# Kernel tuning notes

Measured on AMD Instinct MI355X. Metric: run time of the kernel, lower is better.

Reference implementation:

```python
import jax, jax.numpy as jnp
import numpy as np

B, N, C, E, H, V, T = 64, 196, 512, 512, 1024, 10000, 20
NULL_IDX, START_IDX = 0, 1


def setup_inputs() -> dict:
    key = jax.random.key(0)
    ks = jax.random.split(key, 16)
    p = lambda k, s: jax.random.normal(k, s, jnp.float32) * 0.02
    z = lambda n: jnp.zeros((n,), jnp.float32)
    return dict(
        X=jax.random.normal(ks[0], (B, N, C), jnp.float32),
        emb=p(ks[1], (V, E)),
        W_ih=p(ks[2], (E + C, 4 * H)), b_ih=z(4 * H),
        W_hh=p(ks[3], (H, 4 * H)), b_hh=z(4 * H),
        Wa=p(ks[4], (C, H)), ba=z(H),          # attention lin_annotations
        Wh=p(ks[5], (H, H)), bh=z(H),          # attention lin_hidden
        Wo=p(ks[6], (H, 1)), bo=z(1),          # attention out
        Wlh=p(ks[7], (H, E)), blh=z(E),        # linear_hidden
        Wlc=p(ks[8], (C, E)), blc=z(E),        # linear_context
        Wout=p(ks[9], (E, V)), bout=z(V),      # linear_out
        Wc0=p(ks[10], (C, H)), bc0=z(H),       # cell_init
        Wh0=p(ks[11], (C, H)), bh0=z(H),       # hidden_init
    )


def reference(X, emb, W_ih, b_ih, W_hh, b_hh, Wa, ba, Wh, bh, Wo, bo,
              Wlh, blh, Wlc, blc, Wout, bout, Wc0, bc0, Wh0, bh0):
    Xm = jnp.mean(X, axis=1)                       # [B, C]
    c0 = jnp.tanh(Xm @ Wc0 + bc0)                  # [B, H]
    h0 = jnp.tanh(Xm @ Wh0 + bh0)                  # [B, H]
    Xa = X @ Wa + ba                               # [B, N, H] step-invariant annotation proj
    tok0 = jnp.full((B,), START_IDX, jnp.int32)

    def step(carry, _):
        tok, h, c = carry
        e = emb[tok]                                           # [B, E]
        att = jnp.tanh(Xa + (h @ Wh + bh)[:, None, :])          # [B, N, H]
        # softmax over a size-1 last axis -> weights == 1 (faithful to original)
        w = jax.nn.softmax(att @ Wo + bo, axis=-1)              # [B, N, 1]
        ctx = jnp.sum(w * X, axis=1)                            # [B, C]
        gates = jnp.concatenate([e, ctx], axis=1) @ W_ih + b_ih + h @ W_hh + b_hh
        gi, gf, gg, go = jnp.split(gates, 4, axis=1)            # torch LSTMCell gate order
        c2 = jax.nn.sigmoid(gf) * c + jax.nn.sigmoid(gi) * jnp.tanh(gg)
        h2 = jax.nn.sigmoid(go) * jnp.tanh(c2)
        comb = e + (h2 @ Wlh + blh) + (ctx @ Wlc + blc)         # [B, E]
        lp = jax.nn.log_softmax(comb @ Wout + bout, axis=-1)    # [B, V]
        tok2 = jnp.argmax(lp, axis=-1).astype(jnp.int32)
        return (tok2, h2, c2), lp

    _, lps = jax.lax.scan(step, (tok0, h0, c0), None, length=T - 1)  # [T-1, B, V]
    out0 = jnp.broadcast_to(jax.nn.one_hot(START_IDX, V, dtype=jnp.float32), (B, V))[None]
    out = jnp.concatenate([out0, lps], axis=0)                  # [T, B, V]
    return jnp.transpose(out, (1, 0, 2))                        # [B, T, V]
```

## Files before the change

kernel.cpp:

```cpp
#include <hip/hip_runtime.h>
#include <math.h>

typedef unsigned short u16;
typedef unsigned long long u64;
typedef __attribute__((ext_vector_type(8))) short bf16x8;
typedef __attribute__((ext_vector_type(4))) float f32x4;
typedef __attribute__((ext_vector_type(8))) unsigned short ushort8;

constexpr int kB = 64;
constexpr int kN = 196;
constexpr int kC = 512;
constexpr int kE = 512;
constexpr int kH = 1024;
constexpr int kV = 10000;
constexpr int kT = 20;
constexpr int kG4 = 4 * kH;
constexpr int kKA = 1536;
constexpr int kLT = 625;

__device__ __forceinline__ float sigmoidf_(float x) { return 1.0f / (1.0f + expf(-x)); }

__device__ __forceinline__ u16 f2bf(float x) {
    unsigned u = __float_as_uint(x);
    u += 0x7FFF + ((u >> 16) & 1);
    return (u16)(u >> 16);
}
__device__ __forceinline__ float bf2f(u16 u) {
    return __uint_as_float((unsigned)u << 16);
}
__device__ __forceinline__ void splitbf(float x, u16& hi, u16& lo) {
    hi = f2bf(x);
    lo = f2bf(x - bf2f(hi));
}

__device__ __forceinline__ u64 packMI(float M, int I) {
    unsigned mb = __float_as_uint(M);
    mb = (mb & 0x80000000u) ? ~mb : (mb | 0x80000000u);
    return ((u64)mb << 32) | (u64)(0xFFFFFFFFu - (unsigned)I);
}


__global__ __launch_bounds__(256) void k_colsum(const float* __restrict__ X,
                                                float* __restrict__ XsP) {
    int gid = blockIdx.x * 256 + threadIdx.x;
    int c = gid & 511, b = (gid >> 9) & 63, ch = gid >> 15;
    const float* p = X + (size_t)b * kN * kC + (size_t)(ch * 49) * kC + c;
    float s = 0.f;
    for (int n = 0; n < 49; ++n) s += p[(size_t)n * kC];
    XsP[gid] = s;
}

__global__ __launch_bounds__(256) void k_colred(const float* __restrict__ XsP,
                                                float* __restrict__ XsT) {
    int gid = blockIdx.x * 256 + threadIdx.x;
    int b = gid >> 9, c = gid & 511;
    float s = 0.f;
#pragma unroll
    for (int ch = 0; ch < 4; ++ch) s += XsP[ch * 32768 + b * 512 + c];
    XsT[c * kB + b] = s;
}

__global__ __launch_bounds__(256) void k_setupgemm(const float* __restrict__ XsT,
                                                   const float* __restrict__ W_ih,
                                                   const float* __restrict__ b_ih,
                                                   const float* __restrict__ b_hh,
                                                   const float* __restrict__ Wc0,
                                                   const float* __restrict__ bc0,
                                                   const float* __restrict__ Wh0,
                                                   const float* __restrict__ bh0,
                                                   const float* __restrict__ Wlc,
                                                   const float* __restrict__ blc,
                                                   const float* __restrict__ blh,
                                                   float* __restrict__ gbP,
                                                   float* __restrict__ cBJ,
                                                   u16* __restrict__ hb0Hi,
                                                   u16* __restrict__ hb0Lo,
                                                   float* __restrict__ ctxc) {
    __shared__ float4 wt4[64][8];
    int t = threadIdx.x;
    int b = t & 63, q = t >> 6;
    int tile = blockIdx.x;

    const float* W; const float* bias; float scale; int ldw; int mode; int j;
    if (tile < 128) {
        j = tile * 32; W = W_ih + (size_t)kE * kG4 + j; ldw = kG4;
        bias = nullptr; scale = 1.f; mode = 0;
    } else if (tile < 160) {
        j = (tile - 128) * 32; W = Wc0 + j; ldw = kH;
        bias = bc0 + j; scale = 1.0f / 196.0f; mode = 1;
    } else if (tile < 192) {
        j = (tile - 160) * 32; W = Wh0 + j; ldw = kH;
        bias = bh0 + j; scale = 1.0f / 196.0f; mode = 2;
    } else {
        j = (tile - 192) * 32; W = Wlc + j; ldw = kE;
        bias = blc + j; scale = 1.f; mode = 3;
    }

    int lr = t >> 2, lq2 = (t & 3) * 2;
    float acc[8];
#pragma unroll
    for (int i = 0; i < 8; ++i) acc[i] = 0.f;

    for (int kt = 0; kt < kC; kt += 64) {
        const float* wrow = W + (size_t)(kt + lr) * ldw;
        float4 w0 = *reinterpret_cast<const float4*>(wrow + lq2 * 4);
        float4 w1 = *reinterpret_cast<const float4*>(wrow + lq2 * 4 + 4);
        __syncthreads();
        wt4[lr][lq2] = w0; wt4[lr][lq2 + 1] = w1;
        __syncthreads();
        const float* ap = XsT + (size_t)kt * kB + b;
#pragma unroll 8
        for (int kk = 0; kk < 64; ++kk) {
            float a = ap[kk * 64] * scale;
            float4 u0 = wt4[kk][q * 2];
            float4 u1 = wt4[kk][q * 2 + 1];
            acc[0] += a * u0.x; acc[1] += a * u0.y; acc[2] += a * u0.z; acc[3] += a * u0.w;
            acc[4] += a * u1.x; acc[5] += a * u1.y; acc[6] += a * u1.z; acc[7] += a * u1.w;
        }
    }
#pragma unroll
    for (int cc = 0; cc < 8; ++cc) {
        int col = q * 8 + cc;
        float v = acc[cc];
        if (mode == 0) {
            int jsrc = j + col;
            v += b_ih[jsrc] + b_hh[jsrc];
            int nd = ((jsrc & 1023) << 2) | (jsrc >> 10);
            gbP[(size_t)b * kG4 + nd] = v;
        } else if (mode == 1) {
            v = tanhf(v + bias[col]);
            cBJ[(size_t)b * kH + j + col] = v;
        } else if (mode == 2) {
            v = tanhf(v + bias[col]);
            u16 hi, lo; splitbf(v, hi, lo);
            hb0Hi[(size_t)b * kH + j + col] = hi;
            hb0Lo[(size_t)b * kH + j + col] = lo;
        } else {
            v += bias[col] + blh[j + col];
            ctxc[(size_t)b * kE + j + col] = v;
        }
    }
}

__global__ __launch_bounds__(256) void k_wconv(const float* __restrict__ src,
                                               u16* __restrict__ dhi,
                                               u16* __restrict__ dlo,
                                               int ld, int n_valid, int pitch,
                                               int k_off, int nxTiles) {
    __shared__ float lds[64][65];
    int t = threadIdx.x;
    int nx = blockIdx.x % nxTiles, ky = blockIdx.x / nxTiles;
    int n0 = nx * 64, k0 = ky * 64;
    int c = t & 63, r0 = t >> 6;
#pragma unroll
    for (int i = 0; i < 16; ++i) {
        int r = r0 + i * 4;
        float v = (n0 + c < n_valid) ? src[(size_t)(k0 + r) * ld + n0 + c] : 0.f;
        lds[r][c] = v;
    }
    __syncthreads();
    int nl = t >> 2, kq = t & 3;
#pragma unroll
    for (int half = 0; half < 2; ++half) {
        ushort8 vh, vl;
#pragma unroll
        for (int jj = 0; jj < 8; ++jj) {
            u16 hi, lo; splitbf(lds[kq * 16 + half * 8 + jj][nl], hi, lo);
            vh[jj] = hi; vl[jj] = lo;
        }
        size_t o = (size_t)(n0 + nl) * pitch + k_off + k0 + kq * 16 + half * 8;
        *(ushort8*)(&dhi[o]) = vh;
        *(ushort8*)(&dlo[o]) = vl;
    }
}

__global__ __launch_bounds__(256) void k_wgconv(const float* __restrict__ src,
                                                u16* __restrict__ dhi,
                                                int k_off) {
    __shared__ float lds[64][65];
    int t = threadIdx.x;
    int nx = blockIdx.x & 63, ky = blockIdx.x >> 6;
    int n0 = nx * 64, k0 = ky * 64;
    int c = t & 63, r0 = t >> 6;
#pragma unroll
    for (int i = 0; i < 16; ++i) {
        int r = r0 + i * 4;
        int nd = n0 + c;
        int nsrc = (nd & 3) * 1024 + (nd >> 2);
        lds[r][c] = src[(size_t)(k0 + r) * kG4 + nsrc];
    }
    __syncthreads();
    int nl = t >> 2, kq = t & 3;
#pragma unroll
    for (int half = 0; half < 2; ++half) {
        ushort8 vh;
#pragma unroll
        for (int jj = 0; jj < 8; ++jj) vh[jj] = f2bf(lds[kq * 16 + half * 8 + jj][nl]);
        size_t o = (size_t)(n0 + nl) * kKA + k_off + k0 + kq * 16 + half * 8;
        *(ushort8*)(&dhi[o]) = vh;
    }
}

__global__ __launch_bounds__(256) void k_wconvh(const float* __restrict__ src,
                                                u16* __restrict__ dhi,
                                                int ld, int pitch, int nxTiles) {
    __shared__ float lds[64][65];
    int t = threadIdx.x;
    int nx = blockIdx.x % nxTiles, ky = blockIdx.x / nxTiles;
    int n0 = nx * 64, k0 = ky * 64;
    int c = t & 63, r0 = t >> 6;
#pragma unroll
    for (int i = 0; i < 16; ++i) {
        int r = r0 + i * 4;
        lds[r][c] = src[(size_t)(k0 + r) * ld + n0 + c];
    }
    __syncthreads();
    int nl = t >> 2, kq = t & 3;
#pragma unroll
    for (int half = 0; half < 2; ++half) {
        ushort8 vh;
#pragma unroll
        for (int jj = 0; jj < 8; ++jj) vh[jj] = f2bf(lds[kq * 16 + half * 8 + jj][nl]);
        size_t o = (size_t)(n0 + nl) * pitch + k0 + kq * 16 + half * 8;
        *(ushort8*)(&dhi[o]) = vh;
    }
}

__global__ __launch_bounds__(256) void k_embconv(const float* __restrict__ emb,
                                                 u16* __restrict__ eh,
                                                 u16* __restrict__ el) {
    int gid = blockIdx.x * 256 + threadIdx.x;
    float4 v = *reinterpret_cast<const float4*>(emb + (size_t)gid * 4);
    u16 h0, l0, h1, l1, h2, l2, h3, l3;
    splitbf(v.x, h0, l0); splitbf(v.y, h1, l1);
    splitbf(v.z, h2, l2); splitbf(v.w, h3, l3);
    u64 ph = (u64)h0 | ((u64)h1 << 16) | ((u64)h2 << 32) | ((u64)h3 << 48);
    u64 pl = (u64)l0 | ((u64)l1 << 16) | ((u64)l2 << 32) | ((u64)l3 << 48);
    *reinterpret_cast<u64*>(eh + (size_t)gid * 4) = ph;
    *reinterpret_cast<u64*>(el + (size_t)gid * 4) = pl;
}

__global__ __launch_bounds__(256) void k_out0(float* __restrict__ out) {
    int gid = blockIdx.x * 256 + threadIdx.x;
    if (gid >= kB * kV) return;
    int b = gid / kV, v = gid - b * kV;
    out[(size_t)b * kT * kV + v] = (v == 1) ? 1.0f : 0.0f;
}


struct StepP {
    u16 *hbHi0, *hbLo0, *hbHi1, *hbLo1;
    float *cBJ, *gbP, *ctxc;
    u16 *CbHi, *CbLo;
    const u16 *WgHi, *WlhHi, *WoHi, *WoLo, *embHi, *embLo;
    const float *bout;
    float *lbuf0, *lbuf1;
    float *Ssh;
    u64 *Mxsh;
    float *out;
};

__device__ __forceinline__ int resolveTok(const StepP& p, int step, int b) {
    if (step <= 1) return 1;
    int slot = (step - 1) & 1;
    u64 best = 0;
#pragma unroll
    for (int sh = 0; sh < 8; ++sh) {
        u64 v = p.Mxsh[(slot * 8 + sh) * 64 + b];
        if (v > best) best = v;
    }
    return (int)(0xFFFFFFFFu - (unsigned)(best & 0xFFFFFFFFu));
}

__global__ __launch_bounds__(512) void k_stepG(StepP p, int step) {
    __shared__ float sred[8][64][17];
    __shared__ int tok[64];
    const int blk = blockIdx.x, t = threadIdx.x;
    const int l = t & 63, w = t >> 6, la = l & 15, lg = l >> 4;
    const int Pb = (step - 1) & 1, Qb = step & 1;

    if (t < 64) tok[t] = resolveTok(p, step, t);
    if (blk < 8 && t < 64) {
        int slot = step & 1;
        p.Ssh[(slot * 8 + blk) * 64 + t] = 0.f;
        p.Mxsh[(slot * 8 + blk) * 64 + t] = 0;
    }
    __syncthreads();

    const u16* hpHi = Pb ? p.hbHi1 : p.hbHi0;
    const u16* hpLo = Pb ? p.hbLo1 : p.hbLo0;
    u16* nHi = Qb ? p.hbHi1 : p.hbHi0;
    u16* nLo = Qb ? p.hbLo1 : p.hbLo0;
    const int n0 = blk * 16;
    const int kb = w * 192 + lg * 8;
    const u16* wh = p.WgHi + (size_t)(n0 + la) * kKA + kb;
    int tk[4];
#pragma unroll
    for (int m = 0; m < 4; ++m) tk[m] = tok[m * 16 + la];

    bf16x8 wreg[6];
#pragma unroll
    for (int ks = 0; ks < 6; ++ks) wreg[ks] = *(const bf16x8*)(wh + ks * 32);

    f32x4 acc[4];
#pragma unroll
    for (int m = 0; m < 4; ++m) acc[m] = (f32x4){0.f, 0.f, 0.f, 0.f};
#pragma unroll
    for (int ks = 0; ks < 6; ++ks) {
        int kc = w * 192 + ks * 32;
#pragma unroll
        for (int m = 0; m < 4; ++m) {
            int row = m * 16 + la;
            bf16x8 ahi8, alo8;
            if (kc < kE) {
                size_t o = (size_t)tk[m] * kE + kc + lg * 8;
                ahi8 = *(const bf16x8*)(p.embHi + o);
                alo8 = *(const bf16x8*)(p.embLo + o);
            } else {
                size_t o = (size_t)row * kH + (kc - kE) + lg * 8;
                ahi8 = *(const bf16x8*)(hpHi + o);
                alo8 = *(const bf16x8*)(hpLo + o);
            }
            acc[m] = __builtin_amdgcn_mfma_f32_16x16x32_bf16(ahi8, wreg[ks], acc[m], 0, 0, 0);
            acc[m] = __builtin_amdgcn_mfma_f32_16x16x32_bf16(alo8, wreg[ks], acc[m], 0, 0, 0);
        }
    }
#pragma unroll
    for (int m = 0; m < 4; ++m)
#pragma unroll
        for (int r = 0; r < 4; ++r)
            sred[w][m * 16 + lg * 4 + r][la] = acc[m][r];
    __syncthreads();
    if (t < 256) {
        int b = t & 63, jl = (t >> 6) & 3;
        float g[4];
#pragma unroll
        for (int gi = 0; gi < 4; ++gi) {
            int cc = jl * 4 + gi;
            float s = p.gbP[(size_t)b * kG4 + n0 + cc];
#pragma unroll
            for (int wv = 0; wv < 8; ++wv) s += sred[wv][b][cc];
            g[gi] = s;
        }
        int jp = blk * 4 + jl;
        float cold = p.cBJ[b * kH + jp];
        float c2 = sigmoidf_(g[1]) * cold + sigmoidf_(g[0]) * tanhf(g[2]);
        float h2 = sigmoidf_(g[3]) * tanhf(c2);
        p.cBJ[b * kH + jp] = c2;
        u16 hh, hl; splitbf(h2, hh, hl);
        nHi[(size_t)b * kH + jp] = hh;
        nLo[(size_t)b * kH + jp] = hl;
    }
}

__global__ __launch_bounds__(256) void k_stepC(StepP p, int step) {
    __shared__ float sred[4][64][17];
    __shared__ int tok[64];
    __shared__ float lseArr[64];
    const int blk = blockIdx.x, t = threadIdx.x;
    const int Qb = step & 1;

    if (blk < 32) {
        if (t < 64) tok[t] = resolveTok(p, step, t);
        __syncthreads();
        const u16* hcHi = Qb ? p.hbHi1 : p.hbHi0;
        const u16* hcLo = Qb ? p.hbLo1 : p.hbLo0;
        const int l = t & 63, w = t >> 6, la = l & 15, lg = l >> 4;
        const int n0 = blk * 16;
        const int kb = w * 256 + lg * 8;
        const u16* wh = p.WlhHi + (size_t)(n0 + la) * kH + kb;
        bf16x8 wreg[8];
#pragma unroll
        for (int ks = 0; ks < 8; ++ks) wreg[ks] = *(const bf16x8*)(wh + ks * 32);
        f32x4 acc[4];
#pragma unroll
        for (int m = 0; m < 4; ++m) acc[m] = (f32x4){0.f, 0.f, 0.f, 0.f};
#pragma unroll
        for (int ks = 0; ks < 8; ++ks) {
            int ko = ks * 32;
#pragma unroll
            for (int m = 0; m < 4; ++m) {
                size_t o = (size_t)(m * 16 + la) * kH + kb + ko;
                bf16x8 ahi8 = *(const bf16x8*)(hcHi + o);
                bf16x8 alo8 = *(const bf16x8*)(hcLo + o);
                acc[m] = __builtin_amdgcn_mfma_f32_16x16x32_bf16(ahi8, wreg[ks], acc[m], 0, 0, 0);
                acc[m] = __builtin_amdgcn_mfma_f32_16x16x32_bf16(alo8, wreg[ks], acc[m], 0, 0, 0);
            }
        }
#pragma unroll
        for (int m = 0; m < 4; ++m)
#pragma unroll
            for (int r = 0; r < 4; ++r)
                sred[w][m * 16 + lg * 4 + r][la] = acc[m][r];
        __syncthreads();
        int b = t & 63, cq = t >> 6;
        int tokb = tok[b];
#pragma unroll
        for (int i = 0; i < 4; ++i) {
            int cc = cq * 4 + i;
            int col = (blk * 16) + cc;
            float v = sred[0][b][cc] + sred[1][b][cc] + sred[2][b][cc] + sred[3][b][cc];
            v += bf2f(p.embHi[(size_t)tokb * kE + col]) + bf2f(p.embLo[(size_t)tokb * kE + col]);
            v += p.ctxc[(size_t)b * kE + col];
            u16 hh, hl; splitbf(v, hh, hl);
            p.CbHi[(size_t)b * kE + col] = hh;
            p.CbLo[(size_t)b * kE + col] = hl;
        }
    } else if (step > 1) {
        int slot = (step - 1) & 1;
        if (t < 64) {
            float S = 0.f;
#pragma unroll
            for (int sh = 0; sh < 8; ++sh) S += p.Ssh[(slot * 8 + sh) * 64 + t];
            lseArr[t] = logf(S);
        }
        __syncthreads();
        const float* lb = slot ? p.lbuf1 : p.lbuf0;
        for (int idx = (blk - 32) * 256 + t; idx < kB * kV; idx += 224 * 256) {
            int b = idx / kV, c = idx - b * kV;
            __builtin_nontemporal_store(lb[(size_t)b * kV + c] - lseArr[b],
                                        &p.out[((size_t)b * kT + (step - 1)) * kV + c]);
        }
    }
}

__global__ __launch_bounds__(512) void k_stepL(StepP p, int step) {
    __shared__ float sred[8][64][17];
    __shared__ float redM[256], redS[256];
    __shared__ int redI[256];
    const int blk = blockIdx.x, t = threadIdx.x;
    const int l = t & 63, w = t >> 6, la = l & 15, lg = l >> 4;
    int slot = step & 1;
    float* lb = slot ? p.lbuf1 : p.lbuf0;
    int shard = blk & 7;
    const int c0 = blk * 16;
    const int kb = w * 64 + lg * 8;
    const u16* wh = p.WoHi + (size_t)(c0 + la) * kE + kb;
    const u16* wl = p.WoLo + (size_t)(c0 + la) * kE + kb;
    const u16* a0h = p.CbHi + (size_t)la * kE + kb;
    const u16* a0l = p.CbLo + (size_t)la * kE + kb;

    bf16x8 wh0 = *(const bf16x8*)(wh);
    bf16x8 wh1 = *(const bf16x8*)(wh + 32);
    bf16x8 wl0 = *(const bf16x8*)(wl);
    bf16x8 wl1 = *(const bf16x8*)(wl + 32);

    f32x4 acc[4];
#pragma unroll
    for (int m = 0; m < 4; ++m) acc[m] = (f32x4){0.f, 0.f, 0.f, 0.f};
#pragma unroll
    for (int m = 0; m < 4; ++m) {
        bf16x8 ah0 = *(const bf16x8*)(a0h + (size_t)m * 16 * kE);
        bf16x8 al0 = *(const bf16x8*)(a0l + (size_t)m * 16 * kE);
        bf16x8 ah1 = *(const bf16x8*)(a0h + (size_t)m * 16 * kE + 32);
        bf16x8 al1 = *(const bf16x8*)(a0l + (size_t)m * 16 * kE + 32);
        acc[m] = __builtin_amdgcn_mfma_f32_16x16x32_bf16(ah0, wh0, acc[m], 0, 0, 0);
        acc[m] = __builtin_amdgcn_mfma_f32_16x16x32_bf16(ah0, wl0, acc[m], 0, 0, 0);
        acc[m] = __builtin_amdgcn_mfma_f32_16x16x32_bf16(al0, wh0, acc[m], 0, 0, 0);
        acc[m] = __builtin_amdgcn_mfma_f32_16x16x32_bf16(ah1, wh1, acc[m], 0, 0, 0);
        acc[m] = __builtin_amdgcn_mfma_f32_16x16x32_bf16(ah1, wl1, acc[m], 0, 0, 0);
        acc[m] = __builtin_amdgcn_mfma_f32_16x16x32_bf16(al1, wh1, acc[m], 0, 0, 0);
    }
#pragma unroll
    for (int m = 0; m < 4; ++m)
#pragma unroll
        for (int r = 0; r < 4; ++r)
            sred[w][m * 16 + lg * 4 + r][la] = acc[m][r];
    __syncthreads();
    if (t < 256) {
        int b = t & 63, cq = (t >> 6) & 3;
        float vals[4];
#pragma unroll
        for (int i = 0; i < 4; ++i) {
            int cc = cq * 4 + i;
            float s = p.bout[c0 + cc];
#pragma unroll
            for (int wv = 0; wv < 8; ++wv) s += sred[wv][b][cc];
            vals[i] = s;
        }
        __builtin_nontemporal_store((f32x4){vals[0], vals[1], vals[2], vals[3]},
                                    (f32x4*)(lb + (size_t)b * kV + c0 + cq * 4));
        float m = vals[0]; int mi = 0;
#pragma unroll
        for (int i = 1; i < 4; ++i) if (vals[i] > m) { m = vals[i]; mi = i; }
        float se = 0.f;
#pragma unroll
        for (int i = 0; i < 4; ++i) se += __expf(vals[i] - m);
        redM[t] = m; redS[t] = se; redI[t] = c0 + cq * 4 + mi;
    }
    __syncthreads();
    if (t < 64) {
        float M = redM[t], S = redS[t]; int I = redI[t];
#pragma unroll
        for (int q2 = 1; q2 < 4; ++q2) {
            float m2 = redM[t + q2 * 64], s2 = redS[t + q2 * 64];
            int i2 = redI[t + q2 * 64];
            float Mn = fmaxf(M, m2);
            S = S * __expf(M - Mn) + s2 * __expf(m2 - Mn);
            if (m2 > M || (m2 == M && i2 < I)) I = i2;
            M = Mn;
        }
        float S0 = S * __expf(M);
        atomicAdd(&p.Ssh[(slot * 8 + shard) * 64 + t], S0);
        atomicMax(&p.Mxsh[(slot * 8 + shard) * 64 + t], packMI(M, I));
    }
}

__global__ __launch_bounds__(256) void k_stepO(StepP p) {
    __shared__ float lseArr[64];
    const int blk = blockIdx.x, t = threadIdx.x;
    int slot = (kT - 1) & 1;
    if (t < 64) {
        float S = 0.f;
#pragma unroll
        for (int sh = 0; sh < 8; ++sh) S += p.Ssh[(slot * 8 + sh) * 64 + t];
        lseArr[t] = logf(S);
    }
    __syncthreads();
    const float* lb = slot ? p.lbuf1 : p.lbuf0;
    for (int idx = blk * 256 + t; idx < kB * kV; idx += 256 * 256) {
        int b = idx / kV, c = idx - b * kV;
        __builtin_nontemporal_store(lb[(size_t)b * kV + c] - lseArr[b],
                                    &p.out[((size_t)b * kT + (kT - 1)) * kV + c]);
    }
}


extern "C" void kernel_launch(void* const* d_in, const int* in_sizes, int n_in,
                              void* d_out, int out_size, void* d_ws, size_t ws_size,
                              hipStream_t stream) {
    const float* X    = (const float*)d_in[0];
    const float* emb  = (const float*)d_in[1];
    const float* W_ih = (const float*)d_in[2];
    const float* b_ih = (const float*)d_in[3];
    const float* W_hh = (const float*)d_in[4];
    const float* b_hh = (const float*)d_in[5];
    const float* Wlh  = (const float*)d_in[12];
    const float* blh  = (const float*)d_in[13];
    const float* Wlc  = (const float*)d_in[14];
    const float* blc  = (const float*)d_in[15];
    const float* Wout = (const float*)d_in[16];
    const float* bout = (const float*)d_in[17];
    const float* Wc0  = (const float*)d_in[18];
    const float* bc0  = (const float*)d_in[19];
    const float* Wh0  = (const float*)d_in[20];
    const float* bh0  = (const float*)d_in[21];
    float* out = (float*)d_out;

    char* cur = (char*)d_ws;
    auto carve = [&](size_t bytes) { char* p = cur; cur += (bytes + 255) & ~(size_t)255; return p; };

    u16* hbHi0 = (u16*)carve((size_t)kB * kH * 2);
    u16* hbLo0 = (u16*)carve((size_t)kB * kH * 2);
    u16* hbHi1 = (u16*)carve((size_t)kB * kH * 2);
    u16* hbLo1 = (u16*)carve((size_t)kB * kH * 2);
    float* cBJ  = (float*)carve((size_t)kB * kH * 4);
    float* gbP  = (float*)carve((size_t)kB * kG4 * 4);
    float* ctxc = (float*)carve((size_t)kB * kE * 4);
    u16* CbHi   = (u16*)carve((size_t)kB * kE * 2);
    u16* CbLo   = (u16*)carve((size_t)kB * kE * 2);
    float* XsT  = (float*)carve((size_t)kC * kB * 4);
    float* XsP  = (float*)carve((size_t)4 * kB * kC * 4);
    u16* WgHi   = (u16*)carve((size_t)kG4 * kKA * 2);
    u16* WlhHi  = (u16*)carve((size_t)kE * kH * 2);
    u16* WoHi   = (u16*)carve((size_t)10048 * kE * 2);
    u16* WoLo   = (u16*)carve((size_t)10048 * kE * 2);
    u16* embHi  = (u16*)carve((size_t)10000 * kE * 2);
    u16* embLo  = (u16*)carve((size_t)10000 * kE * 2);
    float* lbuf0 = (float*)carve((size_t)kB * kV * 4);
    float* lbuf1 = (float*)carve((size_t)kB * kV * 4);
    float* Ssh   = (float*)carve((size_t)2 * 8 * 64 * 4);
    u64*   Mxsh  = (u64*)carve((size_t)2 * 8 * 64 * 8);

    k_colsum<<<512, 256, 0, stream>>>(X, XsP);
    k_colred<<<128, 256, 0, stream>>>(XsP, XsT);
    k_setupgemm<<<208, 256, 0, stream>>>(XsT, W_ih, b_ih, b_hh, Wc0, bc0,
                                         Wh0, bh0, Wlc, blc, blh,
                                         gbP, cBJ, hbHi0, hbLo0, ctxc);
    k_out0<<<(kB * kV + 255) / 256, 256, 0, stream>>>(out);
    k_wgconv<<<64 * 8, 256, 0, stream>>>(W_ih, WgHi, 0);
    k_wgconv<<<64 * 16, 256, 0, stream>>>(W_hh, WgHi, kE);
    k_wconvh<<<8 * 16, 256, 0, stream>>>(Wlh, WlhHi, kE, kH, 8);
    k_wconv<<<157 * 8, 256, 0, stream>>>(Wout, WoHi, WoLo, kV, kV, kE, 0, 157);
    k_embconv<<<5000, 256, 0, stream>>>(emb, embHi, embLo);

    StepP sp;
    sp.hbHi0 = hbHi0; sp.hbLo0 = hbLo0; sp.hbHi1 = hbHi1; sp.hbLo1 = hbLo1;
    sp.cBJ = cBJ; sp.gbP = gbP; sp.ctxc = ctxc;
    sp.CbHi = CbHi; sp.CbLo = CbLo;
    sp.WgHi = WgHi; sp.WlhHi = WlhHi;
    sp.WoHi = WoHi; sp.WoLo = WoLo; sp.embHi = embHi; sp.embLo = embLo;
    sp.bout = bout;
    sp.lbuf0 = lbuf0; sp.lbuf1 = lbuf1;
    sp.Ssh = Ssh; sp.Mxsh = Mxsh;
    sp.out = out;

    for (int s = 1; s < kT; ++s) {
        k_stepG<<<256, 512, 0, stream>>>(sp, s);
        k_stepC<<<256, 256, 0, stream>>>(sp, s);
        k_stepL<<<kLT, 512, 0, stream>>>(sp, s);
    }
    k_stepO<<<256, 256, 0, stream>>>(sp);
}
```

Before: 1.023 ms.

## Fuse LSTM gate and combine kernels using a global atomic counter barrier

Merges the per-step gate/LSTM kernel and the combine/output-write kernel into one launch. Blocks finish their gate work and increment a device-wide counter, and the 32 combine blocks spin until all 256 blocks have arrived before reading the new hidden state. This removes one kernel launch and its implicit grid barrier per step, which is 19 launches in total. It depends on all 256 blocks being co-resident, and the spin loop has a bounded timeout that could silently proceed on stale data.

```diff
diff --git a/kernel.cpp b/kernel.cpp
--- a/kernel.cpp
+++ b/kernel.cpp
@@ -37,6 +37,26 @@
     unsigned mb = __float_as_uint(M);
     mb = (mb & 0x80000000u) ? ~mb : (mb | 0x80000000u);
     return ((u64)mb << 32) | (u64)(0xFFFFFFFFu - (unsigned)I);
+}
+
+__device__ __forceinline__ void bumpCtr(int* c) {
+    __syncthreads();
+    if (threadIdx.x == 0) {
+        __builtin_amdgcn_fence(__ATOMIC_RELEASE, "agent");
+        __hip_atomic_fetch_add(c, 1, __ATOMIC_RELAXED, __HIP_MEMORY_SCOPE_AGENT);
+    }
+}
+__device__ __forceinline__ void waitGE(const int* c, int target) {
+    if (threadIdx.x == 0) {
+        int it = 0;
+        while (__hip_atomic_load(c, __ATOMIC_RELAXED, __HIP_MEMORY_SCOPE_AGENT) < target
+               && it < (1 << 20)) {
+            __builtin_amdgcn_s_sleep(8);
+            ++it;
+        }
+        __builtin_amdgcn_fence(__ATOMIC_ACQUIRE, "agent");
+    }
+    __syncthreads();
 }
 
 
@@ -258,6 +278,7 @@
     float *Ssh;
     u64 *Mxsh;
     float *out;
+    int *ctrs;
 };
 
 __device__ __forceinline__ int resolveTok(const StepP& p, int step, int b) {
@@ -272,9 +293,10 @@
     return (int)(0xFFFFFFFFu - (unsigned)(best & 0xFFFFFFFFu));
 }
 
-__global__ __launch_bounds__(512) void k_stepG(StepP p, int step) {
+__global__ __launch_bounds__(512) void k_stepGC(StepP p, int step) {
     __shared__ float sred[8][64][17];
     __shared__ int tok[64];
+    __shared__ float lseArr[64];
     const int blk = blockIdx.x, t = threadIdx.x;
     const int l = t & 63, w = t >> 6, la = l & 15, lg = l >> 4;
     const int Pb = (step - 1) & 1, Qb = step & 1;
@@ -292,91 +314,83 @@
     u16* nHi = Qb ? p.hbHi1 : p.hbHi0;
     u16* nLo = Qb ? p.hbLo1 : p.hbLo0;
     const int n0 = blk * 16;
-    const int kb = w * 192 + lg * 8;
-    const u16* wh = p.WgHi + (size_t)(n0 + la) * kKA + kb;
-    int tk[4];
-#pragma unroll
-    for (int m = 0; m < 4; ++m) tk[m] = tok[m * 16 + la];
-
-    bf16x8 wreg[6];
-#pragma unroll
-    for (int ks = 0; ks < 6; ++ks) wreg[ks] = *(const bf16x8*)(wh + ks * 32);
-
-    f32x4 acc[4];
-#pragma unroll
-    for (int m = 0; m < 4; ++m) acc[m] = (f32x4){0.f, 0.f, 0.f, 0.f};
-#pragma unroll
-    for (int ks = 0; ks < 6; ++ks) {
-        int kc = w * 192 + ks * 32;
-#pragma unroll
-        for (int m = 0; m < 4; ++m) {
-            int row = m * 16 + la;
-            bf16x8 ahi8, alo8;
-            if (kc < kE) {
-                size_t o = (size_t)tk[m] * kE + kc + lg * 8;
-                ahi8 = *(const bf16x8*)(p.embHi + o);
-                alo8 = *(const bf16x8*)(p.embLo + o);
-            } else {
-                size_t o = (size_t)row * kH + (kc - kE) + lg * 8;
-                ahi8 = *(const bf16x8*)(hpHi + o);
-                alo8 = *(const bf16x8*)(hpLo + o);
+    {
+        const int kb = w * 192 + lg * 8;
+        const u16* wh = p.WgHi + (size_t)(n0 + la) * kKA + kb;
+        int tk[4];
+#pragma unroll
+        for (int m = 0; m < 4; ++m) tk[m] = tok[m * 16 + la];
+
+        bf16x8 wreg[6];
+#pragma unroll
+        for (int ks = 0; ks < 6; ++ks) wreg[ks] = *(const bf16x8*)(wh + ks * 32);
+
+        f32x4 acc[4];
+#pragma unroll
+        for (int m = 0; m < 4; ++m) acc[m] = (f32x4){0.f, 0.f, 0.f, 0.f};
+#pragma unroll
+        for (int ks = 0; ks < 6; ++ks) {
+            int kc = w * 192 + ks * 32;
+#pragma unroll
+            for (int m = 0; m < 4; ++m) {
+                int row = m * 16 + la;
+                bf16x8 ahi8, alo8;
+                if (kc < kE) {
+                    size_t o = (size_t)tk[m] * kE + kc + lg * 8;
+                    ahi8 = *(const bf16x8*)(p.embHi + o);
+                    alo8 = *(const bf16x8*)(p.embLo + o);
+                } else {
+                    size_t o = (size_t)row * kH + (kc - kE) + lg * 8;
+                    ahi8 = *(const bf16x8*)(hpHi + o);
+                    alo8 = *(const bf16x8*)(hpLo + o);
+                }
+                acc[m] = __builtin_amdgcn_mfma_f32_16x16x32_bf16(ahi8, wreg[ks], acc[m], 0, 0, 0);
+                acc[m] = __builtin_amdgcn_mfma_f32_16x16x32_bf16(alo8, wreg[ks], acc[m], 0, 0, 0);
             }
-            acc[m] = __builtin_amdgcn_mfma_f32_16x16x32_bf16(ahi8, wreg[ks], acc[m], 0, 0, 0);
-            acc[m] = __builtin_amdgcn_mfma_f32_16x16x32_bf16(alo8, wreg[ks], acc[m], 0, 0, 0);
-        }
-    }
-#pragma unroll
-    for (int m = 0; m < 4; ++m)
-#pragma unroll
-        for (int r = 0; r < 4; ++r)
-            sred[w][m * 16 + lg * 4 + r][la] = acc[m][r];
-    __syncthreads();
-    if (t < 256) {
-        int b = t & 63, jl = (t >> 6) & 3;
-        float g[4];
-#pragma unroll
-        for (int gi = 0; gi < 4; ++gi) {
-            int cc = jl * 4 + gi;
-            float s = p.gbP[(size_t)b * kG4 + n0 + cc];
-#pragma unroll
-            for (int wv = 0; wv < 8; ++wv) s += sred[wv][b][cc];
-            g[gi] = s;
-        }
-        int jp = blk * 4 + jl;
-        float cold = p.cBJ[b * kH + jp];
-        float c2 = sigmoidf_(g[1]) * cold + sigmoidf_(g[0]) * tanhf(g[2]);
-        float h2 = sigmoidf_(g[3]) * tanhf(c2);
-        p.cBJ[b * kH + jp] = c2;
-        u16 hh, hl; splitbf(h2, hh, hl);
-        nHi[(size_t)b * kH + jp] = hh;
-        nLo[(size_t)b * kH + jp] = hl;
-    }
-}
-
-__global__ __launch_bounds__(256) void k_stepC(StepP p, int step) {
-    __shared__ float sred[4][64][17];
-    __shared__ int tok[64];
-    __shared__ float lseArr[64];
-    const int blk = blockIdx.x, t = threadIdx.x;
-    const int Qb = step & 1;
+        }
+#pragma unroll
+        for (int m = 0; m < 4; ++m)
+#pragma unroll
+            for (int r = 0; r < 4; ++r)
+                sred[w][m * 16 + lg * 4 + r][la] = acc[m][r];
+        __syncthreads();
+        if (t < 256) {
+            int b = t & 63, jl = (t >> 6) & 3;
+            float g[4];
+#pragma unroll
+            for (int gi = 0; gi < 4; ++gi) {
+                int cc = jl * 4 + gi;
+                float s = p.gbP[(size_t)b * kG4 + n0 + cc];
+#pragma unroll
+                for (int wv = 0; wv < 8; ++wv) s += sred[wv][b][cc];
+                g[gi] = s;
+            }
+            int jp = blk * 4 + jl;
+            float cold = p.cBJ[b * kH + jp];
+            float c2 = sigmoidf_(g[1]) * cold + sigmoidf_(g[0]) * tanhf(g[2]);
+            float h2 = sigmoidf_(g[3]) * tanhf(c2);
+            p.cBJ[b * kH + jp] = c2;
+            u16 hh, hl; splitbf(h2, hh, hl);
+            nHi[(size_t)b * kH + jp] = hh;
+            nLo[(size_t)b * kH + jp] = hl;
+        }
+    }
+    bumpCtr(p.ctrs);
 
     if (blk < 32) {
-        if (t < 64) tok[t] = resolveTok(p, step, t);
-        __syncthreads();
+        waitGE(p.ctrs, 256 * step);
         const u16* hcHi = Qb ? p.hbHi1 : p.hbHi0;
         const u16* hcLo = Qb ? p.hbLo1 : p.hbLo0;
-        const int l = t & 63, w = t >> 6, la = l & 15, lg = l >> 4;
-        const int n0 = blk * 16;
-        const int kb = w * 256 + lg * 8;
+        const int kb = w * 128 + lg * 8;
         const u16* wh = p.WlhHi + (size_t)(n0 + la) * kH + kb;
-        bf16x8 wreg[8];
-#pragma unroll
-        for (int ks = 0; ks < 8; ++ks) wreg[ks] = *(const bf16x8*)(wh + ks * 32);
+        bf16x8 wreg[4];
+#pragma unroll
+        for (int ks = 0; ks < 4; ++ks) wreg[ks] = *(const bf16x8*)(wh + ks * 32);
         f32x4 acc[4];
 #pragma unroll
         for (int m = 0; m < 4; ++m) acc[m] = (f32x4){0.f, 0.f, 0.f, 0.f};
 #pragma unroll
-        for (int ks = 0; ks < 8; ++ks) {
+        for (int ks = 0; ks < 4; ++ks) {
             int ko = ks * 32;
 #pragma unroll
             for (int m = 0; m < 4; ++m) {
@@ -393,18 +407,22 @@
             for (int r = 0; r < 4; ++r)
                 sred[w][m * 16 + lg * 4 + r][la] = acc[m][r];
         __syncthreads();
-        int b = t & 63, cq = t >> 6;
-        int tokb = tok[b];
-#pragma unroll
-        for (int i = 0; i < 4; ++i) {
-            int cc = cq * 4 + i;
-            int col = (blk * 16) + cc;
-            float v = sred[0][b][cc] + sred[1][b][cc] + sred[2][b][cc] + sred[3][b][cc];
-            v += bf2f(p.embHi[(size_t)tokb * kE + col]) + bf2f(p.embLo[(size_t)tokb * kE + col]);
-            v += p.ctxc[(size_t)b * kE + col];
-            u16 hh, hl; splitbf(v, hh, hl);
-            p.CbHi[(size_t)b * kE + col] = hh;
-            p.CbLo[(size_t)b * kE + col] = hl;
+        if (t < 256) {
+            int b = t & 63, cq = (t >> 6) & 3;
+            int tokb = tok[b];
+#pragma unroll
+            for (int i = 0; i < 4; ++i) {
+                int cc = cq * 4 + i;
+                int col = n0 + cc;
+                float v = 0.f;
+#pragma unroll
+                for (int wv = 0; wv < 8; ++wv) v += sred[wv][b][cc];
+                v += bf2f(p.embHi[(size_t)tokb * kE + col]) + bf2f(p.embLo[(size_t)tokb * kE + col]);
+                v += p.ctxc[(size_t)b * kE + col];
+                u16 hh, hl; splitbf(v, hh, hl);
+                p.CbHi[(size_t)b * kE + col] = hh;
+                p.CbLo[(size_t)b * kE + col] = hl;
+            }
         }
     } else if (step > 1) {
         int slot = (step - 1) & 1;
@@ -416,7 +434,7 @@
         }
         __syncthreads();
         const float* lb = slot ? p.lbuf1 : p.lbuf0;
-        for (int idx = (blk - 32) * 256 + t; idx < kB * kV; idx += 224 * 256) {
+        for (int idx = (blk - 32) * 512 + t; idx < kB * kV; idx += 224 * 512) {
             int b = idx / kV, c = idx - b * kV;
             __builtin_nontemporal_store(lb[(size_t)b * kV + c] - lseArr[b],
                                         &p.out[((size_t)b * kT + (step - 1)) * kV + c]);
@@ -571,6 +589,9 @@
     float* lbuf1 = (float*)carve((size_t)kB * kV * 4);
     float* Ssh   = (float*)carve((size_t)2 * 8 * 64 * 4);
     u64*   Mxsh  = (u64*)carve((size_t)2 * 8 * 64 * 8);
+    int*   ctrs  = (int*)carve(256);
+
+    hipMemsetAsync(ctrs, 0, 256, stream);
 
     k_colsum<<<512, 256, 0, stream>>>(X, XsP);
     k_colred<<<128, 256, 0, stream>>>(XsP, XsT);
@@ -594,10 +615,10 @@
     sp.lbuf0 = lbuf0; sp.lbuf1 = lbuf1;
     sp.Ssh = Ssh; sp.Mxsh = Mxsh;
     sp.out = out;
+    sp.ctrs = ctrs;
 
     for (int s = 1; s < kT; ++s) {
-        k_stepG<<<256, 512, 0, stream>>>(sp, s);
-        k_stepC<<<256, 256, 0, stream>>>(sp, s);
+        k_stepGC<<<256, 512, 0, stream>>>(sp, s);
         k_stepL<<<kLT, 512, 0, stream>>>(sp, s);
     }
     k_stepO<<<256, 256, 0, stream>>>(sp);
```

After: 1.251 ms. 22.2% more time.

## Merge weight-prep launches into one kernel and write logits directly into output

Applied to the files above, without the earlier changes.

Six setup kernels (weight bf16 conversions, embedding split, first-row init) are folded into a single k_prep launch that dispatches on block index, cutting launch overhead. The step kernel also writes raw logits straight into the output tensor instead of a double-buffered scratch, and the later normalisation pass reads them back in place and subtracts the log-sum-exp. This removes the two scratch buffers and a separate read stream. In exchange the output is written twice and read once per step, and correctness relies on the in-place row not being touched by other work in between.

```diff
diff --git a/kernel.cpp b/kernel.cpp
--- a/kernel.cpp
+++ b/kernel.cpp
@@ -142,44 +142,12 @@
     }
 }
 
-__global__ __launch_bounds__(256) void k_wconv(const float* __restrict__ src,
-                                               u16* __restrict__ dhi,
-                                               u16* __restrict__ dlo,
-                                               int ld, int n_valid, int pitch,
-                                               int k_off, int nxTiles) {
-    __shared__ float lds[64][65];
+typedef float LdsT[64][65];
+
+__device__ __forceinline__ void wgconv_body(LdsT& lds, const float* __restrict__ src,
+                                            u16* __restrict__ dhi, int k_off, int bid) {
     int t = threadIdx.x;
-    int nx = blockIdx.x % nxTiles, ky = blockIdx.x / nxTiles;
-    int n0 = nx * 64, k0 = ky * 64;
-    int c = t & 63, r0 = t >> 6;
-#pragma unroll
-    for (int i = 0; i < 16; ++i) {
-        int r = r0 + i * 4;
-        float v = (n0 + c < n_valid) ? src[(size_t)(k0 + r) * ld + n0 + c] : 0.f;
-        lds[r][c] = v;
-    }
-    __syncthreads();
-    int nl = t >> 2, kq = t & 3;
-#pragma unroll
-    for (int half = 0; half < 2; ++half) {
-        ushort8 vh, vl;
-#pragma unroll
-        for (int jj = 0; jj < 8; ++jj) {
-            u16 hi, lo; splitbf(lds[kq * 16 + half * 8 + jj][nl], hi, lo);
-            vh[jj] = hi; vl[jj] = lo;
-        }
-        size_t o = (size_t)(n0 + nl) * pitch + k_off + k0 + kq * 16 + half * 8;
-        *(ushort8*)(&dhi[o]) = vh;
-        *(ushort8*)(&dlo[o]) = vl;
-    }
-}
-
-__global__ __launch_bounds__(256) void k_wgconv(const float* __restrict__ src,
-                                                u16* __restrict__ dhi,
-                                                int k_off) {
-    __shared__ float lds[64][65];
-    int t = threadIdx.x;
-    int nx = blockIdx.x & 63, ky = blockIdx.x >> 6;
+    int nx = bid & 63, ky = bid >> 6;
     int n0 = nx * 64, k0 = ky * 64;
     int c = t & 63, r0 = t >> 6;
 #pragma unroll
@@ -201,12 +169,11 @@
     }
 }
 
-__global__ __launch_bounds__(256) void k_wconvh(const float* __restrict__ src,
-                                                u16* __restrict__ dhi,
-                                                int ld, int pitch, int nxTiles) {
-    __shared__ float lds[64][65];
+__device__ __forceinline__ void wconvh_body(LdsT& lds, const float* __restrict__ src,
+                                            u16* __restrict__ dhi, int ld, int pitch,
+                                            int nxTiles, int bid) {
     int t = threadIdx.x;
-    int nx = blockIdx.x % nxTiles, ky = blockIdx.x / nxTiles;
+    int nx = bid % nxTiles, ky = bid / nxTiles;
     int n0 = nx * 64, k0 = ky * 64;
     int c = t & 63, r0 = t >> 6;
 #pragma unroll
@@ -226,25 +193,75 @@
     }
 }
 
-__global__ __launch_bounds__(256) void k_embconv(const float* __restrict__ emb,
-                                                 u16* __restrict__ eh,
-                                                 u16* __restrict__ el) {
-    int gid = blockIdx.x * 256 + threadIdx.x;
-    float4 v = *reinterpret_cast<const float4*>(emb + (size_t)gid * 4);
-    u16 h0, l0, h1, l1, h2, l2, h3, l3;
-    splitbf(v.x, h0, l0); splitbf(v.y, h1, l1);
-    splitbf(v.z, h2, l2); splitbf(v.w, h3, l3);
-    u64 ph = (u64)h0 | ((u64)h1 << 16) | ((u64)h2 << 32) | ((u64)h3 << 48);
-    u64 pl = (u64)l0 | ((u64)l1 << 16) | ((u64)l2 << 32) | ((u64)l3 << 48);
-    *reinterpret_cast<u64*>(eh + (size_t)gid * 4) = ph;
-    *reinterpret_cast<u64*>(el + (size_t)gid * 4) = pl;
-}
-
-__global__ __launch_bounds__(256) void k_out0(float* __restrict__ out) {
-    int gid = blockIdx.x * 256 + threadIdx.x;
-    if (gid >= kB * kV) return;
-    int b = gid / kV, v = gid - b * kV;
-    out[(size_t)b * kT * kV + v] = (v == 1) ? 1.0f : 0.0f;
+__device__ __forceinline__ void wconv_body(LdsT& lds, const float* __restrict__ src,
+                                           u16* __restrict__ dhi, u16* __restrict__ dlo,
+                                           int ld, int n_valid, int pitch,
+                                           int nxTiles, int bid) {
+    int t = threadIdx.x;
+    int nx = bid % nxTiles, ky = bid / nxTiles;
+    int n0 = nx * 64, k0 = ky * 64;
+    int c = t & 63, r0 = t >> 6;
+#pragma unroll
+    for (int i = 0; i < 16; ++i) {
+        int r = r0 + i * 4;
+        float v = (n0 + c < n_valid) ? src[(size_t)(k0 + r) * ld + n0 + c] : 0.f;
+        lds[r][c] = v;
+    }
+    __syncthreads();
+    int nl = t >> 2, kq = t & 3;
+#pragma unroll
+    for (int half = 0; half < 2; ++half) {
+        ushort8 vh, vl;
+#pragma unroll
+        for (int jj = 0; jj < 8; ++jj) {
+            u16 hi, lo; splitbf(lds[kq * 16 + half * 8 + jj][nl], hi, lo);
+            vh[jj] = hi; vl[jj] = lo;
+        }
+        size_t o = (size_t)(n0 + nl) * pitch + k0 + kq * 16 + half * 8;
+        *(ushort8*)(&dhi[o]) = vh;
+        *(ushort8*)(&dlo[o]) = vl;
+    }
+}
+
+__global__ __launch_bounds__(256) void k_prep(const float* __restrict__ W_ih,
+                                              const float* __restrict__ W_hh,
+                                              const float* __restrict__ Wlh,
+                                              const float* __restrict__ Wout,
+                                              const float* __restrict__ emb,
+                                              u16* __restrict__ WgHi,
+                                              u16* __restrict__ WlhHi,
+                                              u16* __restrict__ WoHi,
+                                              u16* __restrict__ WoLo,
+                                              u16* __restrict__ embHi,
+                                              u16* __restrict__ embLo,
+                                              float* __restrict__ out) {
+    __shared__ float lds[64][65];
+    int blk = blockIdx.x, t = threadIdx.x;
+    if (blk < 512) {
+        wgconv_body(lds, W_ih, WgHi, 0, blk);
+    } else if (blk < 1536) {
+        wgconv_body(lds, W_hh, WgHi, kE, blk - 512);
+    } else if (blk < 1664) {
+        wconvh_body(lds, Wlh, WlhHi, kE, kH, 8, blk - 1536);
+    } else if (blk < 2920) {
+        wconv_body(lds, Wout, WoHi, WoLo, kV, kV, kE, 157, blk - 1664);
+    } else if (blk < 7920) {
+        int gid = (blk - 2920) * 256 + t;
+        float4 v = *reinterpret_cast<const float4*>(emb + (size_t)gid * 4);
+        u16 h0, l0, h1, l1, h2, l2, h3, l3;
+        splitbf(v.x, h0, l0); splitbf(v.y, h1, l1);
+        splitbf(v.z, h2, l2); splitbf(v.w, h3, l3);
+        u64 ph = (u64)h0 | ((u64)h1 << 16) | ((u64)h2 << 32) | ((u64)h3 << 48);
+        u64 pl = (u64)l0 | ((u64)l1 << 16) | ((u64)l2 << 32) | ((u64)l3 << 48);
+        *reinterpret_cast<u64*>(embHi + (size_t)gid * 4) = ph;
+        *reinterpret_cast<u64*>(embLo + (size_t)gid * 4) = pl;
+    } else {
+        int gid = (blk - 7920) * 256 + t;
+        if (gid < kB * kV) {
+            int b = gid / kV, v = gid - b * kV;
+            out[(size_t)b * kT * kV + v] = (v == 1) ? 1.0f : 0.0f;
+        }
+    }
 }
 
 
@@ -254,7 +271,6 @@
     u16 *CbHi, *CbLo;
     const u16 *WgHi, *WlhHi, *WoHi, *WoLo, *embHi, *embLo;
     const float *bout;
-    float *lbuf0, *lbuf1;
     float *Ssh;
     u64 *Mxsh;
     float *out;
@@ -415,11 +431,11 @@
             lseArr[t] = logf(S);
         }
         __syncthreads();
-        const float* lb = slot ? p.lbuf1 : p.lbuf0;
         for (int idx = (blk - 32) * 256 + t; idx < kB * kV; idx += 224 * 256) {
             int b = idx / kV, c = idx - b * kV;
-            __builtin_nontemporal_store(lb[(size_t)b * kV + c] - lseArr[b],
-                                        &p.out[((size_t)b * kT + (step - 1)) * kV + c]);
+            float* op = &p.out[((size_t)b * kT + (step - 1)) * kV + c];
+            float v = __builtin_nontemporal_load(op);
+            __builtin_nontemporal_store(v - lseArr[b], op);
         }
     }
 }
@@ -431,7 +447,6 @@
     const int blk = blockIdx.x, t = threadIdx.x;
     const int l = t & 63, w = t >> 6, la = l & 15, lg = l >> 4;
     int slot = step & 1;
-    float* lb = slot ? p.lbuf1 : p.lbuf0;
     int shard = blk & 7;
     const int c0 = blk * 16;
     const int kb = w * 64 + lg * 8;
@@ -479,7 +494,7 @@
             vals[i] = s;
         }
         __builtin_nontemporal_store((f32x4){vals[0], vals[1], vals[2], vals[3]},
-                                    (f32x4*)(lb + (size_t)b * kV + c0 + cq * 4));
+            (f32x4*)(p.out + ((size_t)b * kT + step) * kV + c0 + cq * 4));
         float m = vals[0]; int mi = 0;
 #pragma unroll
         for (int i = 1; i < 4; ++i) if (vals[i] > m) { m = vals[i]; mi = i; }
@@ -517,11 +532,11 @@
         lseArr[t] = logf(S);
     }
     __syncthreads();
-    const float* lb = slot ? p.lbuf1 : p.lbuf0;
     for (int idx = blk * 256 + t; idx < kB * kV; idx += 256 * 256) {
         int b = idx / kV, c = idx - b * kV;
-        __builtin_nontemporal_store(lb[(size_t)b * kV + c] - lseArr[b],
-                                    &p.out[((size_t)b * kT + (kT - 1)) * kV + c]);
+        float* op = &p.out[((size_t)b * kT + (kT - 1)) * kV + c];
+        float v = __builtin_nontemporal_load(op);
+        __builtin_nontemporal_store(v - lseArr[b], op);
     }
 }
 
@@ -567,8 +582,6 @@
     u16* WoLo   = (u16*)carve((size_t)10048 * kE * 2);
     u16* embHi  = (u16*)carve((size_t)10000 * kE * 2);
     u16* embLo  = (u16*)carve((size_t)10000 * kE * 2);
-    float* lbuf0 = (float*)carve((size_t)kB * kV * 4);
-    float* lbuf1 = (float*)carve((size_t)kB * kV * 4);
     float* Ssh   = (float*)carve((size_t)2 * 8 * 64 * 4);
     u64*   Mxsh  = (u64*)carve((size_t)2 * 8 * 64 * 8);
 
@@ -577,12 +590,8 @@
     k_setupgemm<<<208, 256, 0, stream>>>(XsT, W_ih, b_ih, b_hh, Wc0, bc0,
                                          Wh0, bh0, Wlc, blc, blh,
                                          gbP, cBJ, hbHi0, hbLo0, ctxc);
-    k_out0<<<(kB * kV + 255) / 256, 256, 0, stream>>>(out);
-    k_wgconv<<<64 * 8, 256, 0, stream>>>(W_ih, WgHi, 0);
-    k_wgconv<<<64 * 16, 256, 0, stream>>>(W_hh, WgHi, kE);
-    k_wconvh<<<8 * 16, 256, 0, stream>>>(Wlh, WlhHi, kE, kH, 8);
-    k_wconv<<<157 * 8, 256, 0, stream>>>(Wout, WoHi, WoLo, kV, kV, kE, 0, 157);
-    k_embconv<<<5000, 256, 0, stream>>>(emb, embHi, embLo);
+    k_prep<<<10420, 256, 0, stream>>>(W_ih, W_hh, Wlh, Wout, emb,
+                                      WgHi, WlhHi, WoHi, WoLo, embHi, embLo, out);
 
     StepP sp;
     sp.hbHi0 = hbHi0; sp.hbLo0 = hbLo0; sp.hbHi1 = hbHi1; sp.hbLo1 = hbLo1;
@@ -591,7 +600,6 @@
     sp.WgHi = WgHi; sp.WlhHi = WlhHi;
     sp.WoHi = WoHi; sp.WoLo = WoLo; sp.embHi = embHi; sp.embLo = embLo;
     sp.bout = bout;
-    sp.lbuf0 = lbuf0; sp.lbuf1 = lbuf1;
     sp.Ssh = Ssh; sp.Mxsh = Mxsh;
     sp.out = out;
 
```

Result: no change. 1.017 ms (-0.6%).
